# Performance work log

Measured on AMD Instinct MI355X. Metric: run time of the kernel, lower is better.

## Reference

```python
import jax, jax.numpy as jnp
import numpy as np

D_IN = 2048
D_SAE = 16384
BATCH = 4096


def setup_inputs() -> dict:
    key = jax.random.key(0)
    kx, kw, kb, kt, kd = jax.random.split(key, 5)
    x = jax.random.normal(kx, (BATCH, D_IN), dtype=jnp.float32)
    # kaiming-uniform-like init for encoder weight [d_sae, d_in]
    bound = float(np.sqrt(6.0 / D_IN))
    W_enc = jax.random.uniform(kw, (D_SAE, D_IN), minval=-bound, maxval=bound, dtype=jnp.float32)
    b_enc = jnp.zeros((D_SAE,), dtype=jnp.float32)
    # decoder weight [d_in, d_sae]; use small random values instead of the
    # zeros init so the reference output is non-degenerate
    W_dec = jax.random.normal(kd, (D_IN, D_SAE), dtype=jnp.float32) * 0.02
    # learnable per-feature thresholds tau (tau_init=0.0 plus jitter)
    tau = jax.random.normal(kt, (D_SAE,), dtype=jnp.float32) * 0.01
    return {"x": x, "W_enc": W_enc, "b_enc": b_enc, "tau": tau, "W_dec": W_dec, "k_cap": 64}


def reference(x, W_enc, b_enc, tau, W_dec, k_cap):
    # encode: pre = x @ W_enc.T + b_enc  -> [B, d_sae]
    pre = jnp.einsum('bi,si->bs', x, W_enc) + b_enc
    # JumpReLU gate: y = relu(pre - tau), mask = (pre > tau)
    codes = jax.nn.relu(pre - tau)
    mask = (pre > tau).astype(pre.dtype)
    # top-k cap (gate_mode='jumprelu_cap'): keep codes >= k-th largest per row
    k = min(k_cap, codes.shape[1])
    vals = jax.lax.top_k(codes, k)[0]          # [B, k], sorted desc
    kth = vals[:, -1:]                          # [B, 1]
    mask_k = (codes >= kth).astype(codes.dtype)
    codes = codes * mask_k
    mask = mask * mask_k
    # decode: recon = codes @ W_dec.T  -> [B, d_in]
    recon = jnp.einsum('bs,is->bi', codes, W_dec)
    return recon, codes, mask
```

## Files before the change

kernel.cpp:

```cpp
#include <hip/hip_runtime.h>

#define D_IN   2048
#define D_SAE  16384
#define BATCH  4096
#define CAP    256
#define MAXB   64
#define DELTA  1e-2f

typedef __attribute__((ext_vector_type(8))) _Float16 f16x8;
typedef __attribute__((ext_vector_type(4))) _Float16 f16x4;
typedef __attribute__((ext_vector_type(4))) float f32x4;

__global__ __launch_bounds__(256) void to_f16(const float* __restrict__ in,
                                              ushort* __restrict__ out, int n4) {
    int i = blockIdx.x * blockDim.x + threadIdx.x;
    int stride = gridDim.x * blockDim.x;
    for (; i < n4; i += stride) {
        float4 v = ((const float4*)in)[i];
        ushort4 h;
        float*  vp = (float*)&v;
        ushort* hp = (ushort*)&h;
        #pragma unroll
        for (int j = 0; j < 4; ++j) {
            _Float16 f = (_Float16)vp[j];
            hp[j] = *(ushort*)&f;
        }
        ((ushort4*)out)[i] = h;
    }
}

__device__ __forceinline__ void async_copy16(const void* g, void* l) {
    __builtin_amdgcn_global_load_lds(
        (const __attribute__((address_space(1))) unsigned int*)g,
        (__attribute__((address_space(3))) unsigned int*)l, 16, 0, 0);
}

template<int F16OUT>
__global__ __launch_bounds__(512) void gemm_enc_mfma(
        const ushort* __restrict__ xh,
        const ushort* __restrict__ wh,
        const float* __restrict__ b_enc,
        const float* __restrict__ tau,
        void* __restrict__ rawout) {
    __shared__ ushort lds[2][2][2][8192];

    const int tid  = threadIdx.x;
    const int w    = tid >> 6;
    const int lane = tid & 63;
    const int wm   = w >> 2;
    const int wn   = w & 3;
    const int m0 = blockIdx.x * 256;
    const int s0 = blockIdx.y * 256;

    const int fr = lane & 15;
    const int fq = lane >> 4;

    const int srow0 = w * 8 + (lane >> 3);
    const int srow1 = 64 + srow0;
    const int sc0i  = ((lane & 7) - srow0 & 7) * 8;

    const ushort* panelA = xh + (size_t)m0 * 2048;
    const ushort* panelB = wh + (size_t)s0 * 2048;

    auto stage_half = [&](int bufi, int ab, int h, int koff) {
        const ushort* gp = (ab == 0) ? panelA : panelB;
        const ushort* g0 = gp + (size_t)(h * 128 + srow0) * 2048 + koff + sc0i;
        const ushort* g1 = gp + (size_t)(h * 128 + srow1) * 2048 + koff + sc0i;
        async_copy16(g0, &lds[bufi][ab][h][w * 512]);
        async_copy16(g1, &lds[bufi][ab][h][4096 + w * 512]);
    };

    int a_off[8][2], b_off[4][2];
    #pragma unroll
    for (int m = 0; m < 8; ++m) {
        int r = m * 16 + fr;
        #pragma unroll
        for (int kk = 0; kk < 2; ++kk)
            a_off[m][kk] = r * 64 + (((kk * 4 + fq) + r) & 7) * 8;
    }
    #pragma unroll
    for (int g = 0; g < 4; ++g) {
        int r = (wn & 1) * 64 + g * 16 + fr;
        #pragma unroll
        for (int kk = 0; kk < 2; ++kk)
            b_off[g][kk] = r * 64 + (((kk * 4 + fq) + r) & 7) * 8;
    }

    f32x4 acc[8][4] = {};

    stage_half(0, 0, 0, 0);
    stage_half(0, 0, 1, 0);
    stage_half(0, 1, 0, 0);
    stage_half(0, 1, 1, 0);
    asm volatile("s_waitcnt vmcnt(0)" ::: "memory");
    asm volatile("s_barrier" ::: "memory");

#define PHASE(QM, QN, AB, H)                                                   \
    do {                                                                       \
        if (t < 31) stage_half(nbuf, AB, H, knext);                            \
        f16x8 af[4][2], bf[2][2];                                              \
        _Pragma("unroll") for (int mm = 0; mm < 4; ++mm)                       \
            _Pragma("unroll") for (int kk = 0; kk < 2; ++kk)                   \
                af[mm][kk] = *(const f16x8*)&ldsA[a_off[(QM) * 4 + mm][kk]];   \
        _Pragma("unroll") for (int nn = 0; nn < 2; ++nn)                       \
            _Pragma("unroll") for (int kk = 0; kk < 2; ++kk)                   \
                bf[nn][kk] = *(const f16x8*)&ldsB[b_off[(QN) * 2 + nn][kk]];   \
        asm volatile("s_barrier" ::: "memory");                                \
        __builtin_amdgcn_s_setprio(1);                                         \
        _Pragma("unroll") for (int kk = 0; kk < 2; ++kk)                       \
            _Pragma("unroll") for (int mm = 0; mm < 4; ++mm)                   \
                _Pragma("unroll") for (int nn = 0; nn < 2; ++nn)               \
                    acc[(QM) * 4 + mm][(QN) * 2 + nn] =                        \
                        __builtin_amdgcn_mfma_f32_16x16x32_f16(                \
                            af[mm][kk], bf[nn][kk],                            \
                            acc[(QM) * 4 + mm][(QN) * 2 + nn], 0, 0, 0);       \
        __builtin_amdgcn_s_setprio(0);                                         \
        asm volatile("s_barrier" ::: "memory");                                \
    } while (0)

    for (int t = 0; t < 32; ++t) {
        const int cbuf = t & 1, nbuf = cbuf ^ 1;
        const int knext = (t + 1) * 64;
        const ushort* ldsA = &lds[cbuf][0][wm][0];
        const ushort* ldsB = &lds[cbuf][1][wn >> 1][0];
        PHASE(0, 0, 0, 0);
        PHASE(0, 1, 0, 1);
        PHASE(1, 0, 1, 0);
        PHASE(1, 1, 1, 1);
        asm volatile("s_waitcnt vmcnt(0)" ::: "memory");
        asm volatile("s_barrier" ::: "memory");
    }
#undef PHASE

    float bias[4];
    int col[4];
    #pragma unroll
    for (int n = 0; n < 4; ++n) {
        col[n] = s0 + wn * 64 + n * 16 + fr;
        bias[n] = b_enc[col[n]] - tau[col[n]];
    }
    #pragma unroll
    for (int m = 0; m < 8; ++m) {
        int rbase = m0 + wm * 128 + m * 16 + fq * 4;
        #pragma unroll
        for (int n = 0; n < 4; ++n) {
            #pragma unroll
            for (int r = 0; r < 4; ++r) {
                float v = fmaxf(acc[m][n][r] + bias[n], 0.f);
                size_t ofs = (size_t)(rbase + r) * D_SAE + col[n];
                if (F16OUT) {
                    _Float16 hv = (_Float16)v;
                    ((ushort*)rawout)[ofs] = *(ushort*)&hv;
                } else {
                    ((float*)rawout)[ofs] = v;
                }
            }
        }
    }
}

__global__ __launch_bounds__(256) void transpose_wdec_f16(const float* __restrict__ W_dec,
                                                          _Float16* __restrict__ W_decT) {
    __shared__ float t[64][65];
    const int tid = threadIdx.x;
    const int x0 = blockIdx.x * 64;
    const int y0 = blockIdx.y * 64;
    const int tx = tid & 15;
    const int ty = tid >> 4;
    #pragma unroll
    for (int p = 0; p < 4; ++p) {
        float4 v = *(const float4*)&W_dec[(size_t)(y0 + p * 16 + ty) * D_SAE + x0 + tx * 4];
        t[p * 16 + ty][tx * 4 + 0] = v.x;
        t[p * 16 + ty][tx * 4 + 1] = v.y;
        t[p * 16 + ty][tx * 4 + 2] = v.z;
        t[p * 16 + ty][tx * 4 + 3] = v.w;
    }
    __syncthreads();
    #pragma unroll
    for (int p = 0; p < 4; ++p) {
        int s = p * 16 + ty;
        f16x4 o;
        #pragma unroll
        for (int q = 0; q < 4; ++q)
            o[q] = (_Float16)t[tx * 4 + q][s];
        *(f16x4*)&W_decT[(size_t)(x0 + s) * D_IN + y0 + tx * 4] = o;
    }
}

template<int SRC16>
__global__ __launch_bounds__(256) void select_apply(
        const void* __restrict__ rawsrc,
        float* __restrict__ codes, float* __restrict__ mask,
        const int* __restrict__ kptr,
        const float* __restrict__ x, const float* __restrict__ W_enc,
        const float* __restrict__ b_enc, const float* __restrict__ tau,
        int* __restrict__ cnt_out, int* __restrict__ idx_out,
        float* __restrict__ val_out) {
    const int row = blockIdx.x;
    const int tid = threadIdx.x;
    const long base = (long)row * D_SAE;

    float c[8][8];
    if (SRC16) {
        const ushort* rh = (const ushort*)rawsrc;
        #pragma unroll
        for (int i = 0; i < 8; ++i) {
            uint4 u = *(const uint4*)(rh + base + i * 2048 + tid * 8);
            const unsigned* up = (const unsigned*)&u;
            #pragma unroll
            for (int q = 0; q < 4; ++q) {
                ushort b0 = (ushort)(up[q] & 0xFFFFu), b1 = (ushort)(up[q] >> 16);
                _Float16 h0, h1;
                *(ushort*)&h0 = b0; *(ushort*)&h1 = b1;
                c[i][2 * q]     = (float)h0;
                c[i][2 * q + 1] = (float)h1;
            }
        }
    } else {
        const float* rf = (const float*)rawsrc;
        #pragma unroll
        for (int i = 0; i < 8; ++i) {
            float4 v0 = *(const float4*)(rf + base + i * 2048 + tid * 8);
            float4 v1 = *(const float4*)(rf + base + i * 2048 + tid * 8 + 4);
            c[i][0] = v0.x; c[i][1] = v0.y; c[i][2] = v0.z; c[i][3] = v0.w;
            c[i][4] = v1.x; c[i][5] = v1.y; c[i][6] = v1.z; c[i][7] = v1.w;
        }
    }

    int K = kptr[0];
    if (K > D_SAE) K = D_SAE;

    __shared__ int    hist[1024];
    __shared__ int    scan[256];
    __shared__ int    wsum[4];
    __shared__ int    bidx[MAXB];
    __shared__ double exactv[MAXB];
    __shared__ int    selfl[MAXB];
    __shared__ double dsum[4];
    __shared__ int    sh_B, sh_nAB, sh_kpat;

    #pragma unroll
    for (int q = 0; q < 4; ++q) hist[tid + q * 256] = 0;
    if (tid == 0) { sh_B = -1; sh_nAB = 0; }
    __syncthreads();
    #pragma unroll
    for (int i = 0; i < 8; ++i)
        #pragma unroll
        for (int j = 0; j < 8; ++j) {
            _Float16 h = (_Float16)c[i][j];
            ushort pat = *(ushort*)&h;
            if (pat) atomicAdd(&hist[pat >> 6], 1);
        }
    __syncthreads();

    int s_loc = hist[4 * tid] + hist[4 * tid + 1] + hist[4 * tid + 2] + hist[4 * tid + 3];
    const int my = 255 - tid;
    scan[my] = s_loc;
    __syncthreads();
    #pragma unroll
    for (int off = 1; off < 256; off <<= 1) {
        int a = scan[my];
        int b = (my >= off) ? scan[my - off] : 0;
        __syncthreads();
        scan[my] = a + b;
        __syncthreads();
    }
    int I = scan[my];
    int E = I - s_loc;
    if (I >= K && E < K) {
        int cnt = E, b;
        for (b = 4 * tid + 3; b > 4 * tid; --b) {
            cnt += hist[b];
            if (cnt >= K) break;
        }
        if (cnt < K) { cnt += hist[4 * tid]; b = 4 * tid; }
        sh_B = b;
        sh_nAB = cnt - hist[b];
    }
    __syncthreads();
    const int B = sh_B, nAB = sh_nAB;

    if (tid < 64) hist[tid] = 0;
    __syncthreads();
    if (B >= 0) {
        #pragma unroll
        for (int i = 0; i < 8; ++i)
            #pragma unroll
            for (int j = 0; j < 8; ++j) {
                _Float16 h = (_Float16)c[i][j];
                ushort pat = *(ushort*)&h;
                if (pat && (int)(pat >> 6) == B) atomicAdd(&hist[pat & 63], 1);
            }
    }
    __syncthreads();
    if (tid == 0) {
        int kpat = 0;
        if (B >= 0) {
            int cnt = nAB, l;
            for (l = 63; l >= 0; --l) {
                cnt += hist[l];
                if (cnt >= K) break;
            }
            if (l < 0) l = 0;
            kpat = (B << 6) | l;
        }
        sh_kpat = kpat;
    }
    __syncthreads();
    _Float16 kh; *(ushort*)&kh = (ushort)sh_kpat;
    const float kf = (float)kh;
    const float thr_hi = kf + DELTA;
    const float thr_lo = kf - DELTA;

    int cA = 0, cB2 = 0;
    #pragma unroll
    for (int i = 0; i < 8; ++i)
        #pragma unroll
        for (int j = 0; j < 8; ++j) {
            float cc = c[i][j];
            cA  += (cc > thr_hi);
            cB2 += (cc >= thr_lo) && (cc <= thr_hi);
        }
    {
        int a = cA;
        #pragma unroll
        for (int off = 32; off; off >>= 1) a += __shfl_xor(a, off, 64);
        if ((tid & 63) == 0) wsum[tid >> 6] = a;
    }
    __syncthreads();
    const int nA = wsum[0] + wsum[1] + wsum[2] + wsum[3];
    __syncthreads();

    scan[tid] = cB2;
    __syncthreads();
    #pragma unroll
    for (int off = 1; off < 256; off <<= 1) {
        int a = scan[tid];
        int b = (tid >= off) ? scan[tid - off] : 0;
        __syncthreads();
        scan[tid] = a + b;
        __syncthreads();
    }
    int posB = scan[tid] - cB2;
    int nb   = scan[255];
    if (nb > MAXB) nb = MAXB;

    {
        int p = posB;
        #pragma unroll
        for (int i = 0; i < 8; ++i)
            #pragma unroll
            for (int j = 0; j < 8; ++j) {
                float cc = c[i][j];
                if ((cc >= thr_lo) && (cc <= thr_hi)) {
                    if (p < MAXB) bidx[p] = i * 2048 + tid * 8 + j;
                    ++p;
                }
            }
    }
    __syncthreads();

    const float* xrow = x + (size_t)row * D_IN;
    for (int jj = 0; jj < nb; ++jj) {
        int s = bidx[jj];
        const float* wrow = W_enc + (size_t)s * D_IN;
        double a = 0.0;
        #pragma unroll
        for (int q = 0; q < 8; ++q)
            a += (double)xrow[tid * 8 + q] * (double)wrow[tid * 8 + q];
        #pragma unroll
        for (int off = 32; off; off >>= 1) a += __shfl_xor(a, off, 64);
        if ((tid & 63) == 0) dsum[tid >> 6] = a;
        __syncthreads();
        if (tid == 0)
            exactv[jj] = dsum[0] + dsum[1] + dsum[2] + dsum[3]
                         + (double)b_enc[s] - (double)tau[s];
        __syncthreads();
    }

    int m = K - nA;
    if (m > nb) m = nb;
    if (tid < nb) {
        double e = exactv[tid];
        int rank = 0;
        for (int l = 0; l < nb; ++l) rank += (exactv[l] > e);
        selfl[tid] = (rank < m) ? 1 : 0;
    }
    __syncthreads();

    unsigned long long ov = 0ull;
    for (int jj = 0; jj < nb; ++jj) {
        int s = bidx[jj];
        if (((s >> 3) & 255) == tid && selfl[jj])
            ov |= 1ull << (((s >> 11) << 3) | (s & 7));
    }

    int kc = 0;
    #pragma unroll
    for (int i = 0; i < 8; ++i)
        #pragma unroll
        for (int j = 0; j < 8; ++j) {
            float cc = c[i][j];
            bool sel = (cc > thr_hi) || ((ov >> (i * 8 + j)) & 1ull);
            kc += sel && (cc > 0.f);
        }
    __syncthreads();
    scan[tid] = kc;
    __syncthreads();
    #pragma unroll
    for (int off = 1; off < 256; off <<= 1) {
        int a = scan[tid];
        int b = (tid >= off) ? scan[tid - off] : 0;
        __syncthreads();
        scan[tid] = a + b;
        __syncthreads();
    }
    int pos   = scan[tid] - kc;
    int total = scan[255];

    #pragma unroll
    for (int i = 0; i < 8; ++i) {
        f32x4 cf0, cf1, mf0, mf1;
        #pragma unroll
        for (int j = 0; j < 8; ++j) {
            float cc = c[i][j];
            bool sel = (cc > thr_hi) || ((ov >> (i * 8 + j)) & 1ull);
            bool m_  = sel && (cc > 0.f);
            float cv = sel ? cc : 0.f;
            float mv = m_ ? 1.f : 0.f;
            if (j < 4) { cf0[j] = cv; mf0[j] = mv; }
            else       { cf1[j - 4] = cv; mf1[j - 4] = mv; }
            if (m_) {
                if (pos < CAP) {
                    idx_out[row * CAP + pos] = i * 2048 + tid * 8 + j;
                    val_out[row * CAP + pos] = cv;
                }
                ++pos;
            }
        }
        long o = base + i * 2048 + tid * 8;
        __builtin_nontemporal_store(cf0, (f32x4*)(codes + o));
        __builtin_nontemporal_store(cf1, (f32x4*)(codes + o + 4));
        __builtin_nontemporal_store(mf0, (f32x4*)(mask + o));
        __builtin_nontemporal_store(mf1, (f32x4*)(mask + o + 4));
    }
    if (tid == 0) cnt_out[row] = total < CAP ? total : CAP;
}

__global__ __launch_bounds__(256) void recon_sparse(const _Float16* __restrict__ Wd16,
                                                    const int* __restrict__ cnt,
                                                    const int* __restrict__ idx,
                                                    const float* __restrict__ val,
                                                    float* __restrict__ recon) {
    const int row = blockIdx.x;
    const int tid = threadIdx.x;
    __shared__ int   s_idx[CAP];
    __shared__ float s_val[CAP];
    const int n = cnt[row];
    for (int j = tid; j < n; j += 256) {
        s_idx[j] = idx[row * CAP + j];
        s_val[j] = val[row * CAP + j];
    }
    __syncthreads();

    float4 a0 = {0.f, 0.f, 0.f, 0.f};
    float4 a1 = {0.f, 0.f, 0.f, 0.f};
    for (int j = 0; j < n; ++j) {
        float c = s_val[j];
        const _Float16* w = Wd16 + (size_t)s_idx[j] * D_IN;
        f16x4 w0 = *(const f16x4*)(w + tid * 4);
        f16x4 w1 = *(const f16x4*)(w + 1024 + tid * 4);
        a0.x = fmaf(c, (float)w0[0], a0.x); a0.y = fmaf(c, (float)w0[1], a0.y);
        a0.z = fmaf(c, (float)w0[2], a0.z); a0.w = fmaf(c, (float)w0[3], a0.w);
        a1.x = fmaf(c, (float)w1[0], a1.x); a1.y = fmaf(c, (float)w1[1], a1.y);
        a1.z = fmaf(c, (float)w1[2], a1.z); a1.w = fmaf(c, (float)w1[3], a1.w);
    }
    float* out = recon + (size_t)row * D_IN;
    *(float4*)(out + tid * 4)        = a0;
    *(float4*)(out + 1024 + tid * 4) = a1;
}

extern "C" void kernel_launch(void* const* d_in, const int* in_sizes, int n_in,
                              void* d_out, int out_size, void* d_ws, size_t ws_size,
                              hipStream_t stream) {
    const float* x     = (const float*)d_in[0];
    const float* W_enc = (const float*)d_in[1];
    const float* b_enc = (const float*)d_in[2];
    const float* tau   = (const float*)d_in[3];
    const float* W_dec = (const float*)d_in[4];
    const int*   kptr  = (const int*)d_in[5];

    float* recon = (float*)d_out;
    float* codes = recon + (size_t)BATCH * D_IN;
    float* maskp = codes + (size_t)BATCH * D_SAE;

    char* w = (char*)d_ws;
    const size_t OFF_X   = (size_t)D_SAE * D_IN * 2;
    const size_t OFF_RAW = OFF_X + (size_t)BATCH * D_IN * 2;
    const size_t RAWSZ   = (size_t)BATCH * D_SAE * 2;
    const size_t TAILSZ  = 16384 + 2 * (size_t)BATCH * CAP * 4;
    const bool f16raw = ws_size >= OFF_RAW + RAWSZ + TAILSZ;

    const size_t OFF_CNT = f16raw ? (OFF_RAW + RAWSZ) : OFF_RAW;
    ushort*   w_f16  = (ushort*)w;
    ushort*   x_f16  = (ushort*)(w + OFF_X);
    _Float16* W_decT = (_Float16*)w;
    int*      cnt    = (int*)  (w + OFF_CNT);
    int*      idxl   = (int*)  (w + OFF_CNT + 16384);
    float*    vall   = (float*)(w + OFF_CNT + 16384 + (size_t)BATCH * CAP * 4);
    void*     raw    = f16raw ? (void*)(w + OFF_RAW) : (void*)codes;

    hipLaunchKernelGGL(to_f16, dim3(1024), dim3(256), 0, stream,
                       x, x_f16, BATCH * D_IN / 4);
    hipLaunchKernelGGL(to_f16, dim3(4096), dim3(256), 0, stream,
                       W_enc, w_f16, D_SAE * D_IN / 4);
    if (f16raw) {
        hipLaunchKernelGGL((gemm_enc_mfma<1>), dim3(BATCH / 256, D_SAE / 256), dim3(512), 0, stream,
                           x_f16, w_f16, b_enc, tau, raw);
        hipLaunchKernelGGL((select_apply<1>), dim3(BATCH), dim3(256), 0, stream,
                           raw, codes, maskp, kptr, x, W_enc, b_enc, tau, cnt, idxl, vall);
    } else {
        hipLaunchKernelGGL((gemm_enc_mfma<0>), dim3(BATCH / 256, D_SAE / 256), dim3(512), 0, stream,
                           x_f16, w_f16, b_enc, tau, raw);
        hipLaunchKernelGGL((select_apply<0>), dim3(BATCH), dim3(256), 0, stream,
                           raw, codes, maskp, kptr, x, W_enc, b_enc, tau, cnt, idxl, vall);
    }
    hipLaunchKernelGGL(transpose_wdec_f16, dim3(D_SAE / 64, D_IN / 64), dim3(256), 0, stream,
                       W_dec, W_decT);
    hipLaunchKernelGGL(recon_sparse, dim3(BATCH), dim3(256), 0, stream,
                       W_decT, cnt, idxl, vall, recon);
}
```

Before: 701.8 us.

## Issue all next-tile async loads upfront and split sparse recon across two thread teams

In the encoder GEMM, the four async global-to-LDS copies for the next k-tile are now issued together at the start of each iteration instead of being spread one per compute phase. The aim is to get all prefetches in flight earlier, at the cost of a burst of memory traffic and a different overlap pattern with the MFMA phases. The sparse reconstruction kernel now uses 512 threads, with two teams each accumulating alternate nonzero features. The teams' partial sums are combined through shared memory and written with nontemporal stores. This adds more loads in flight per row, paid for with an extra LDS reduction and a barrier.

```diff
diff --git a/kernel.cpp b/kernel.cpp
--- a/kernel.cpp
+++ b/kernel.cpp
@@ -57,7 +57,7 @@
 
     const int srow0 = w * 8 + (lane >> 3);
     const int srow1 = 64 + srow0;
-    const int sc0i  = ((lane & 7) - srow0 & 7) * 8;
+    const int sc0i  = (((lane & 7) - srow0) & 7) * 8;
 
     const ushort* panelA = xh + (size_t)m0 * 2048;
     const ushort* panelB = wh + (size_t)s0 * 2048;
@@ -95,9 +95,8 @@
     asm volatile("s_waitcnt vmcnt(0)" ::: "memory");
     asm volatile("s_barrier" ::: "memory");
 
-#define PHASE(QM, QN, AB, H)                                                   \
+#define PHASE(QM, QN)                                                          \
     do {                                                                       \
-        if (t < 31) stage_half(nbuf, AB, H, knext);                            \
         f16x8 af[4][2], bf[2][2];                                              \
         _Pragma("unroll") for (int mm = 0; mm < 4; ++mm)                       \
             _Pragma("unroll") for (int kk = 0; kk < 2; ++kk)                   \
@@ -123,10 +122,16 @@
         const int knext = (t + 1) * 64;
         const ushort* ldsA = &lds[cbuf][0][wm][0];
         const ushort* ldsB = &lds[cbuf][1][wn >> 1][0];
-        PHASE(0, 0, 0, 0);
-        PHASE(0, 1, 0, 1);
-        PHASE(1, 0, 1, 0);
-        PHASE(1, 1, 1, 1);
+        if (t < 31) {
+            stage_half(nbuf, 0, 0, knext);
+            stage_half(nbuf, 0, 1, knext);
+            stage_half(nbuf, 1, 0, knext);
+            stage_half(nbuf, 1, 1, knext);
+        }
+        PHASE(0, 0);
+        PHASE(0, 1);
+        PHASE(1, 0);
+        PHASE(1, 1);
         asm volatile("s_waitcnt vmcnt(0)" ::: "memory");
         asm volatile("s_barrier" ::: "memory");
     }
@@ -447,17 +452,20 @@
     if (tid == 0) cnt_out[row] = total < CAP ? total : CAP;
 }
 
-__global__ __launch_bounds__(256) void recon_sparse(const _Float16* __restrict__ Wd16,
+__global__ __launch_bounds__(512) void recon_sparse(const _Float16* __restrict__ Wd16,
                                                     const int* __restrict__ cnt,
                                                     const int* __restrict__ idx,
                                                     const float* __restrict__ val,
                                                     float* __restrict__ recon) {
-    const int row = blockIdx.x;
-    const int tid = threadIdx.x;
+    const int row  = blockIdx.x;
+    const int tid  = threadIdx.x;
+    const int team = tid >> 8;
+    const int lt   = tid & 255;
     __shared__ int   s_idx[CAP];
     __shared__ float s_val[CAP];
+    __shared__ float part[2048];
     const int n = cnt[row];
-    for (int j = tid; j < n; j += 256) {
+    for (int j = tid; j < n; j += 512) {
         s_idx[j] = idx[row * CAP + j];
         s_val[j] = val[row * CAP + j];
     }
@@ -465,19 +473,31 @@
 
     float4 a0 = {0.f, 0.f, 0.f, 0.f};
     float4 a1 = {0.f, 0.f, 0.f, 0.f};
-    for (int j = 0; j < n; ++j) {
+    #pragma unroll 2
+    for (int j = team; j < n; j += 2) {
         float c = s_val[j];
         const _Float16* w = Wd16 + (size_t)s_idx[j] * D_IN;
-        f16x4 w0 = *(const f16x4*)(w + tid * 4);
-        f16x4 w1 = *(const f16x4*)(w + 1024 + tid * 4);
+        f16x4 w0 = *(const f16x4*)(w + lt * 4);
+        f16x4 w1 = *(const f16x4*)(w + 1024 + lt * 4);
         a0.x = fmaf(c, (float)w0[0], a0.x); a0.y = fmaf(c, (float)w0[1], a0.y);
         a0.z = fmaf(c, (float)w0[2], a0.z); a0.w = fmaf(c, (float)w0[3], a0.w);
         a1.x = fmaf(c, (float)w1[0], a1.x); a1.y = fmaf(c, (float)w1[1], a1.y);
         a1.z = fmaf(c, (float)w1[2], a1.z); a1.w = fmaf(c, (float)w1[3], a1.w);
     }
-    float* out = recon + (size_t)row * D_IN;
-    *(float4*)(out + tid * 4)        = a0;
-    *(float4*)(out + 1024 + tid * 4) = a1;
+    if (team == 1) {
+        *(float4*)&part[lt * 4]        = a0;
+        *(float4*)&part[1024 + lt * 4] = a1;
+    }
+    __syncthreads();
+    if (team == 0) {
+        float4 p0 = *(const float4*)&part[lt * 4];
+        float4 p1 = *(const float4*)&part[1024 + lt * 4];
+        a0.x += p0.x; a0.y += p0.y; a0.z += p0.z; a0.w += p0.w;
+        a1.x += p1.x; a1.y += p1.y; a1.z += p1.z; a1.w += p1.w;
+        float* out = recon + (size_t)row * D_IN;
+        __builtin_nontemporal_store(*(f32x4*)&a0, (f32x4*)(out + lt * 4));
+        __builtin_nontemporal_store(*(f32x4*)&a1, (f32x4*)(out + 1024 + lt * 4));
+    }
 }
 
 extern "C" void kernel_launch(void* const* d_in, const int* in_sizes, int n_in,
@@ -527,6 +547,6 @@
     }
     hipLaunchKernelGGL(transpose_wdec_f16, dim3(D_SAE / 64, D_IN / 64), dim3(256), 0, stream,
                        W_dec, W_decT);
-    hipLaunchKernelGGL(recon_sparse, dim3(BATCH), dim3(256), 0, stream,
+    hipLaunchKernelGGL(recon_sparse, dim3(BATCH), dim3(512), 0, stream,
                        W_decT, cnt, idxl, vall, recon);
 }
```

After: 727.4 us. 1.04x slower.

## Restructure encoder GEMM staging into k-half chunks with vmcnt-gated pipelining

Applied to the files above, without the earlier changes.

Changes the encoder GEMM's LDS layout from a row-swizzled tile to a k-chunk-major layout indexed by 8-element column chunks. Global-to-LDS staging is split into two 32-wide k-halves that are issued one ahead of compute. Each sub-iteration now waits with a partial vmcnt and a single barrier, then runs a full 8x4 MFMA burst, replacing four phases with two barriers each. The aim is fewer barriers and better overlap of async copies with MFMA work. The trade-off is that the swizzle, which avoided LDS bank conflicts, is dropped, and correctness now depends on the vmcnt accounting.

```diff
diff --git a/kernel.cpp b/kernel.cpp
--- a/kernel.cpp
+++ b/kernel.cpp
@@ -42,7 +42,7 @@
         const float* __restrict__ b_enc,
         const float* __restrict__ tau,
         void* __restrict__ rawout) {
-    __shared__ ushort lds[2][2][2][8192];
+    __shared__ ushort lds[2][2][2][4][2048];
 
     const int tid  = threadIdx.x;
     const int w    = tid >> 6;
@@ -55,82 +55,59 @@
     const int fr = lane & 15;
     const int fq = lane >> 4;
 
-    const int srow0 = w * 8 + (lane >> 3);
-    const int srow1 = 64 + srow0;
-    const int sc0i  = ((lane & 7) - srow0 & 7) * 8;
+    const int sc   = tid >> 8;
+    const int srow = tid & 255;
 
     const ushort* panelA = xh + (size_t)m0 * 2048;
     const ushort* panelB = wh + (size_t)s0 * 2048;
 
-    auto stage_half = [&](int bufi, int ab, int h, int koff) {
-        const ushort* gp = (ab == 0) ? panelA : panelB;
-        const ushort* g0 = gp + (size_t)(h * 128 + srow0) * 2048 + koff + sc0i;
-        const ushort* g1 = gp + (size_t)(h * 128 + srow1) * 2048 + koff + sc0i;
-        async_copy16(g0, &lds[bufi][ab][h][w * 512]);
-        async_copy16(g1, &lds[bufi][ab][h][4096 + w * 512]);
+    auto stage_kh = [&](int bufi, int kh, int koff) {
+        #pragma unroll
+        for (int q = 0; q < 2; ++q) {
+            int c = q * 2 + sc;
+            async_copy16(panelA + (size_t)srow * 2048 + koff + c * 8,
+                         &lds[bufi][0][kh][c][srow * 8]);
+            async_copy16(panelB + (size_t)srow * 2048 + koff + c * 8,
+                         &lds[bufi][1][kh][c][srow * 8]);
+        }
     };
 
-    int a_off[8][2], b_off[4][2];
-    #pragma unroll
-    for (int m = 0; m < 8; ++m) {
-        int r = m * 16 + fr;
-        #pragma unroll
-        for (int kk = 0; kk < 2; ++kk)
-            a_off[m][kk] = r * 64 + (((kk * 4 + fq) + r) & 7) * 8;
-    }
-    #pragma unroll
-    for (int g = 0; g < 4; ++g) {
-        int r = (wn & 1) * 64 + g * 16 + fr;
-        #pragma unroll
-        for (int kk = 0; kk < 2; ++kk)
-            b_off[g][kk] = r * 64 + (((kk * 4 + fq) + r) & 7) * 8;
-    }
-
     f32x4 acc[8][4] = {};
 
-    stage_half(0, 0, 0, 0);
-    stage_half(0, 0, 1, 0);
-    stage_half(0, 1, 0, 0);
-    stage_half(0, 1, 1, 0);
-    asm volatile("s_waitcnt vmcnt(0)" ::: "memory");
-    asm volatile("s_barrier" ::: "memory");
-
-#define PHASE(QM, QN, AB, H)                                                   \
+    stage_kh(0, 0, 0);
+    stage_kh(0, 1, 32);
+
+#define SUBITER(KH, VM)                                                        \
     do {                                                                       \
-        if (t < 31) stage_half(nbuf, AB, H, knext);                            \
-        f16x8 af[4][2], bf[2][2];                                              \
-        _Pragma("unroll") for (int mm = 0; mm < 4; ++mm)                       \
-            _Pragma("unroll") for (int kk = 0; kk < 2; ++kk)                   \
-                af[mm][kk] = *(const f16x8*)&ldsA[a_off[(QM) * 4 + mm][kk]];   \
-        _Pragma("unroll") for (int nn = 0; nn < 2; ++nn)                       \
-            _Pragma("unroll") for (int kk = 0; kk < 2; ++kk)                   \
-                bf[nn][kk] = *(const f16x8*)&ldsB[b_off[(QN) * 2 + nn][kk]];   \
+        asm volatile("s_waitcnt vmcnt(" #VM ")" ::: "memory");                 \
         asm volatile("s_barrier" ::: "memory");                                \
+        f16x8 af[8], bf[4];                                                    \
+        _Pragma("unroll") for (int m = 0; m < 8; ++m)                          \
+            af[m] = *(const f16x8*)&lds[cbuf][0][KH][fq][(wm * 128 + m * 16 + fr) * 8]; \
+        _Pragma("unroll") for (int g = 0; g < 4; ++g)                          \
+            bf[g] = *(const f16x8*)&lds[cbuf][1][KH][fq][(wn * 64 + g * 16 + fr) * 8];  \
         __builtin_amdgcn_s_setprio(1);                                         \
-        _Pragma("unroll") for (int kk = 0; kk < 2; ++kk)                       \
-            _Pragma("unroll") for (int mm = 0; mm < 4; ++mm)                   \
-                _Pragma("unroll") for (int nn = 0; nn < 2; ++nn)               \
-                    acc[(QM) * 4 + mm][(QN) * 2 + nn] =                        \
-                        __builtin_amdgcn_mfma_f32_16x16x32_f16(                \
-                            af[mm][kk], bf[nn][kk],                            \
-                            acc[(QM) * 4 + mm][(QN) * 2 + nn], 0, 0, 0);       \
+        _Pragma("unroll") for (int m = 0; m < 8; ++m)                          \
+            _Pragma("unroll") for (int g = 0; g < 4; ++g)                      \
+                acc[m][g] = __builtin_amdgcn_mfma_f32_16x16x32_f16(            \
+                    af[m], bf[g], acc[m][g], 0, 0, 0);                         \
         __builtin_amdgcn_s_setprio(0);                                         \
-        asm volatile("s_barrier" ::: "memory");                                \
     } while (0)
 
-    for (int t = 0; t < 32; ++t) {
+    for (int t = 0; t < 31; ++t) {
         const int cbuf = t & 1, nbuf = cbuf ^ 1;
         const int knext = (t + 1) * 64;
-        const ushort* ldsA = &lds[cbuf][0][wm][0];
-        const ushort* ldsB = &lds[cbuf][1][wn >> 1][0];
-        PHASE(0, 0, 0, 0);
-        PHASE(0, 1, 0, 1);
-        PHASE(1, 0, 1, 0);
-        PHASE(1, 1, 1, 1);
-        asm volatile("s_waitcnt vmcnt(0)" ::: "memory");
-        asm volatile("s_barrier" ::: "memory");
-    }
-#undef PHASE
+        stage_kh(nbuf, 0, knext);
+        SUBITER(0, 8);
+        stage_kh(nbuf, 1, knext + 32);
+        SUBITER(1, 8);
+    }
+    {
+        const int cbuf = 31 & 1;
+        SUBITER(0, 4);
+        SUBITER(1, 0);
+    }
+#undef SUBITER
 
     float bias[4];
     int col[4];
```

After: 965.9 us. 37.6% more time.
